# Optimization experiments

Hardware: AMD Instinct MI355X
Metric: run time of the kernel (lower is better)

The kernel has to match this reference:

```python
import jax, jax.numpy as jnp
import numpy as np

DELTA_VAR = 0.5
DELTA_DIST = 1.5
PULL_W = 1.0
PUSH_W = 1.0
REG_W = 0.001
IGNORE_INDEX = 255
NUM_IDS = 16  # max instance id used in setup; fixed segment count for jit


def setup_inputs() -> dict:
    key = jax.random.key(0)
    k1, k2 = jax.random.split(key)
    B, D, H, W = 8, 32, 512, 512
    pred_embedding = jax.random.normal(k1, (B, D, H, W), dtype=jnp.float32)
    gt_instance = jax.random.randint(k2, (B, H, W), 0, NUM_IDS).astype(jnp.int32)
    valid_mask = jnp.ones((B, H, W), dtype=bool)
    return {"pred_embedding": pred_embedding, "gt_instance": gt_instance, "valid_mask": valid_mask}


def _per_image(emb_hwd, inst_hw, vmask_hw):
    # emb_hwd: [H, W, D]; inst_hw, vmask_hw: [H, W]
    D = emb_hwd.shape[-1]
    e = emb_hwd.reshape(-1, D)                       # [N, D]
    inst = inst_hw.reshape(-1)
    m = (vmask_hw.reshape(-1)) & (inst != IGNORE_INDEX)
    mf = m.astype(e.dtype)
    # route invalid pixels to dummy segment NUM_IDS
    seg = jnp.where(m, inst, NUM_IDS)
    counts = jax.ops.segment_sum(mf, seg, num_segments=NUM_IDS + 1)[:NUM_IDS]      # [K]
    sums = jax.ops.segment_sum(e * mf[:, None], seg, num_segments=NUM_IDS + 1)[:NUM_IDS]  # [K, D]
    valid_id = counts > 0
    n_ids = jnp.sum(valid_id.astype(e.dtype))
    centers = sums / jnp.maximum(counts, 1.0)[:, None]                              # [K, D]
    # ---- pull: per-instance mean of relu(||pix - center|| - delta_var)^2 ----
    centers_full = jnp.concatenate([centers, jnp.zeros((1, D), e.dtype)], axis=0)   # dummy row
    c_pix = centers_full[seg]                                                        # [N, D]
    sq = jnp.sum((e - c_pix) ** 2, axis=-1)
    dist = jnp.sqrt(jnp.where(m, sq, 1.0))
    val = jnp.where(m, jax.nn.relu(dist - DELTA_VAR) ** 2, 0.0)
    per_inst = jax.ops.segment_sum(val, seg, num_segments=NUM_IDS + 1)[:NUM_IDS] / jnp.maximum(counts, 1.0)
    pull = jnp.sum(per_inst * valid_id.astype(e.dtype)) / jnp.maximum(n_ids, 1.0)
    # ---- push: pairwise relu(2*delta_dist - ||ci - cj||)^2, off-diagonal mean ----
    sqm = jnp.sum((centers[:, None, :] - centers[None, :, :]) ** 2, axis=-1)        # [K, K]
    eye = jnp.eye(NUM_IDS, dtype=bool)
    pmask = valid_id[:, None] & valid_id[None, :] & (~eye)
    dm = jnp.sqrt(jnp.where(pmask, sqm, 1.0))
    push_mat = jax.nn.relu(2.0 * DELTA_DIST - dm) ** 2
    n_pairs = jnp.sum(pmask.astype(e.dtype))
    push = jnp.where(n_ids > 1.0, jnp.sum(jnp.where(pmask, push_mat, 0.0)) / jnp.maximum(n_pairs, 1.0), 0.0)
    # ---- reg: mean center norm ----
    csq = jnp.sum(centers ** 2, axis=-1)
    cnorm = jnp.sqrt(jnp.where(valid_id, csq, 1.0))
    reg = jnp.sum(jnp.where(valid_id, cnorm, 0.0)) / jnp.maximum(n_ids, 1.0)
    vb = jnp.any(m).astype(e.dtype)
    return pull * vb, push * vb, reg * vb, vb


def reference(pred_embedding, gt_instance, valid_mask):
    emb = jnp.transpose(pred_embedding, (0, 2, 3, 1))  # [B, H, W, D]
    pulls, pushes, regs, vbs = jax.vmap(_per_image)(emb, gt_instance, valid_mask)
    nvb = jnp.sum(vbs)
    denom = jnp.maximum(nvb, 1.0)
    loss = (PULL_W * jnp.sum(pulls) + PUSH_W * jnp.sum(pushes) + REG_W * jnp.sum(regs)) / denom
    return jnp.where(nvb > 0, loss, 0.0)
```

## Files before the change

kernel.cpp:

```cpp
#include <hip/hip_runtime.h>

typedef _Float16 half4 __attribute__((ext_vector_type(4)));
typedef float f32x4 __attribute__((ext_vector_type(4)));

#define NB 8
#define ND 32
#define NHW (512*512)
#define NK 16
#define IGN 255

#define WS_S   1088
#define O_CNT  0
#define O_VPIX 16
#define O_SUM  32
#define O_PULL 1056

#define IDP_OFF 65536

#define ATPB 256
#define ABLK 128
#define TILE 128
#define NTILES 16

#define PTPB 256
#define PCHUNKS 256
#define PPIX (NHW / PCHUNKS)

__global__ __launch_bounds__(256) void k_zero(float* __restrict__ ws) {
    int i = blockIdx.x * blockDim.x + threadIdx.x;
    if (i < NB * WS_S) ws[i] = 0.f;
}

__global__ __launch_bounds__(ATPB) void k_accum(const float* __restrict__ pred,
                                                const int* __restrict__ inst,
                                                const unsigned char* __restrict__ msk,
                                                float* __restrict__ ws,
                                                unsigned char* __restrict__ idp) {
    __shared__ __align__(16) float buf[2][ND][TILE];
    __shared__ float lcnt[2][NK + 1];
    const int tid = threadIdx.x;
    const int w = tid >> 6, l = tid & 63;
    const int dgrp = w & 1;
    const int phalf = w >> 1;
    const int b = blockIdx.y, chunk = blockIdx.x;

    if (tid < 2 * (NK + 1)) ((float*)lcnt)[tid] = 0.f;

    const size_t img = (size_t)b * NHW;
    const float* pb = pred + (size_t)b * ND * NHW;
    const int base0 = chunk * (NTILES * TILE);

#define STAGE(CUR, T)                                                          \
    {                                                                          \
        const int tb_ = base0 + (T) * TILE;                                    \
        _Pragma("unroll")                                                      \
        for (int q_ = 0; q_ < 4; ++q_) {                                       \
            const int r0_ = 8 * w + 2 * q_;                                    \
            const int r_ = r0_ + (l >> 5);                                     \
            const int col_ = 4 * ((l & 31) ^ (r_ & 7));                        \
            const float* src_ = pb + (size_t)r_ * NHW + tb_ + col_;            \
            __builtin_amdgcn_global_load_lds(                                  \
                (const __attribute__((address_space(1))) unsigned*)src_,       \
                (__attribute__((address_space(3))) unsigned*)&buf[CUR][r0_][0],\
                16, 0, 0);                                                     \
        }                                                                      \
    }

#define LOADIDS(IV, MV, TB)                                                    \
    if (l < 16) {                                                              \
        (IV) = *(const int4*)(inst + img + (TB) + phalf * 64 + 4 * l);         \
        (MV) = *(const unsigned*)(msk + img + (TB) + phalf * 64 + 4 * l);      \
    }

#define DECODE(IV, MV, PK, VC)                                                 \
    if (l < 16) {                                                              \
        const int ia_[4] = {(IV).x, (IV).y, (IV).z, (IV).w};                   \
        (PK) = 0u;                                                             \
        _Pragma("unroll")                                                      \
        for (int p_ = 0; p_ < 4; ++p_) {                                       \
            const bool m_ = ((((MV) >> (8 * p_)) & 0xffu) != 0u) &&            \
                            (ia_[p_] != IGN);                                  \
            if (dgrp == 0) (VC) += m_ ? 1.f : 0.f;                             \
            const unsigned s_ =                                                \
                (m_ && (unsigned)ia_[p_] < NK) ? (unsigned)ia_[p_] : NK;       \
            (PK) |= s_ << (8 * p_);                                            \
        }                                                                      \
    }

    int4 iv; unsigned mv = 0;
    LOADIDS(iv, mv, base0);
    STAGE(0, 0);
    unsigned pk = 0;
    float vcnt = 0.f;
    DECODE(iv, mv, pk, vcnt);
    __syncthreads();

    f32x4 acc = {0.f, 0.f, 0.f, 0.f};
    for (int t = 0; t < NTILES; ++t) {
        const int cur = t & 1;
        const int tb = base0 + t * TILE;
        int4 iv2; unsigned mv2 = 0;
        if (t + 1 < NTILES) {
            LOADIDS(iv2, mv2, base0 + (t + 1) * TILE);
            STAGE(cur ^ 1, t + 1);
        }
        if (dgrp == 0 && l < 16) {
            uchar4 pkb = {(unsigned char)(pk & 0xff),
                          (unsigned char)((pk >> 8) & 0xff),
                          (unsigned char)((pk >> 16) & 0xff),
                          (unsigned char)(pk >> 24)};
            *(uchar4*)(idp + img + tb + phalf * 64 + 4 * l) = pkb;
            #pragma unroll
            for (int p = 0; p < 4; ++p)
                atomicAdd(&lcnt[phalf][(pk >> (8 * p)) & 0xffu], 1.f);
        }
        #pragma unroll
        for (int kk = 0; kk < 4; ++kk) {
            const int row = dgrp * 16 + (l & 15);
            const int cb = phalf * 16 + kk * 4 + (l >> 4);
            const f32x4 av = *(const f32x4*)
                (&buf[cur][0][0] + row * TILE + 4 * (cb ^ (row & 7)));
            half4 ah;
            #pragma unroll
            for (int e = 0; e < 4; ++e) ah[e] = (_Float16)av[e];
            const int srcl = kk * 4 + (l >> 4);
            const unsigned pkk = (unsigned)__shfl((int)pk, srcl);
            half4 bh;
            #pragma unroll
            for (int e = 0; e < 4; ++e)
                bh[e] = (((pkk >> (8 * e)) & 0xffu) == (unsigned)(l & 15))
                            ? (_Float16)1.f : (_Float16)0.f;
            acc = __builtin_amdgcn_mfma_f32_16x16x16f16(ah, bh, acc, 0, 0, 0);
        }
        iv = iv2; mv = mv2;
        DECODE(iv, mv, pk, vcnt);
        __syncthreads();
    }
#undef STAGE
#undef LOADIDS
#undef DECODE

    float* sc = &buf[0][0][0];
    const int widx = dgrp * 2 + phalf;
    #pragma unroll
    for (int r = 0; r < 4; ++r)
        sc[(widx * 16 + 4 * (l >> 4) + r) * 16 + (l & 15)] = acc[r];
    __syncthreads();

    float* wb = ws + b * WS_S;
    for (int i = tid; i < NK * ND; i += ATPB) {
        const int k = i >> 5, d = i & 31, dg = d >> 4, dr = d & 15;
        const float v = sc[((dg * 2 + 0) * 16 + dr) * 16 + k] +
                        sc[((dg * 2 + 1) * 16 + dr) * 16 + k];
        atomicAdd(&wb[O_SUM + i], v);
    }
    if (tid < NK) atomicAdd(&wb[O_CNT + tid], lcnt[0][tid] + lcnt[1][tid]);
    if (w == 0 || w == 2) {
        #pragma unroll
        for (int off = 8; off > 0; off >>= 1) vcnt += __shfl_down(vcnt, off);
        if (l == 0) atomicAdd(&wb[O_VPIX], vcnt);
    }
}

__global__ __launch_bounds__(PTPB) void k_pull(const float* __restrict__ pred,
                                               const unsigned char* __restrict__ idp,
                                               float* __restrict__ ws) {
    __shared__ float lc[17][ND + 1];
    __shared__ float lcc[NK];
    __shared__ float lp[2][NK];
    const int tid = threadIdx.x;
    const int b = NB - 1 - blockIdx.y;
    const int chunk = PCHUNKS - 1 - blockIdx.x;
    const int half = (tid >> 5) & 1;
    float* wb = ws + b * WS_S;

    if (tid < NK) lcc[tid] = wb[O_CNT + tid];
    if (tid < 2 * NK) ((float*)lp)[tid] = 0.f;
    __syncthreads();
    for (int i = tid; i < 17 * ND; i += PTPB)
        lc[i >> 5][i & 31] =
            (i < NK * ND) ? wb[O_SUM + i] / fmaxf(lcc[i >> 5], 1.f) : 0.f;
    __syncthreads();

    const size_t img = (size_t)b * NHW;
    const float* pb = pred + (size_t)b * ND * NHW;

    const int pix = chunk * PPIX + 4 * tid;
    const unsigned pk = *(const unsigned*)(idp + img + pix);
    const int id[4] = {(int)(pk & 0xff), (int)((pk >> 8) & 0xff),
                       (int)((pk >> 16) & 0xff), (int)(pk >> 24)};
    float sq[4] = {0.f, 0.f, 0.f, 0.f};
    #pragma unroll 8
    for (int d = 0; d < ND; ++d) {
        const float4 v = *(const float4*)(pb + (size_t)d * NHW + pix);
        float df0 = v.x - lc[id[0]][d];
        float df1 = v.y - lc[id[1]][d];
        float df2 = v.z - lc[id[2]][d];
        float df3 = v.w - lc[id[3]][d];
        sq[0] += df0 * df0; sq[1] += df1 * df1;
        sq[2] += df2 * df2; sq[3] += df3 * df3;
    }
    #pragma unroll
    for (int p = 0; p < 4; ++p) {
        if (id[p] < NK) {
            float r = fmaxf(sqrtf(sq[p]) - 0.5f, 0.f);
            atomicAdd(&lp[half][id[p]], r * r);
        }
    }
    __syncthreads();
    if (tid < NK) atomicAdd(&wb[O_PULL + tid], lp[0][tid] + lp[1][tid]);
}

__global__ void k_final(const float* __restrict__ ws, float* __restrict__ out) {
    __shared__ float lc[NK][ND];
    __shared__ float lcc[NK];
    const int tid = threadIdx.x;
    float total = 0.f, nvb = 0.f;

    for (int b = 0; b < NB; ++b) {
        const float* wb = ws + b * WS_S;
        if (tid < NK) lcc[tid] = wb[O_CNT + tid];
        __syncthreads();
        for (int i = tid; i < NK * ND; i += 64)
            lc[i >> 5][i & 31] = wb[O_SUM + i] / fmaxf(lcc[i >> 5], 1.f);
        __syncthreads();

        float nids_p = (tid < NK && lcc[tid] > 0.f) ? 1.f : 0.f;
        float pull_p = (tid < NK && lcc[tid] > 0.f)
                           ? wb[O_PULL + tid] / fmaxf(lcc[tid], 1.f) : 0.f;
        float reg_p = 0.f;
        if (tid < NK && lcc[tid] > 0.f) {
            float cs = 0.f;
            for (int d = 0; d < ND; ++d) cs += lc[tid][d] * lc[tid][d];
            reg_p = sqrtf(cs);
        }
        float push_p = 0.f;
        #pragma unroll
        for (int q = 0; q < 4; ++q) {
            const int p = 4 * tid + q, i = p >> 4, j = p & 15;
            if (i != j && lcc[i] > 0.f && lcc[j] > 0.f) {
                float sq2 = 0.f;
                for (int d = 0; d < ND; ++d) {
                    float df = lc[i][d] - lc[j][d];
                    sq2 += df * df;
                }
                float r = fmaxf(3.f - sqrtf(sq2), 0.f);
                push_p += r * r;
            }
        }
        #pragma unroll
        for (int off = 32; off > 0; off >>= 1) {
            nids_p += __shfl_down(nids_p, off);
            pull_p += __shfl_down(pull_p, off);
            reg_p  += __shfl_down(reg_p, off);
            push_p += __shfl_down(push_p, off);
        }
        if (tid == 0) {
            const float nids = nids_p;
            const float pull = pull_p / fmaxf(nids, 1.f);
            const float npairs = nids * nids - nids;
            const float push =
                (nids > 1.f) ? push_p / fmaxf(npairs, 1.f) : 0.f;
            const float reg = reg_p / fmaxf(nids, 1.f);
            const float vb = (wb[O_VPIX] > 0.f) ? 1.f : 0.f;
            total += (pull + push + 0.001f * reg) * vb;
            nvb += vb;
        }
        __syncthreads();
    }
    if (tid == 0) out[0] = (nvb > 0.f) ? total / fmaxf(nvb, 1.f) : 0.f;
}

extern "C" void kernel_launch(void* const* d_in, const int* in_sizes, int n_in,
                              void* d_out, int out_size, void* d_ws, size_t ws_size,
                              hipStream_t stream) {
    const float* pred = (const float*)d_in[0];
    const int* inst = (const int*)d_in[1];
    const unsigned char* msk = (const unsigned char*)d_in[2];
    float* out = (float*)d_out;
    float* ws = (float*)d_ws;
    unsigned char* idp = (unsigned char*)d_ws + IDP_OFF;

    k_zero<<<(NB * WS_S + 255) / 256, 256, 0, stream>>>(ws);
    dim3 agrid(ABLK, NB);
    k_accum<<<agrid, ATPB, 0, stream>>>(pred, inst, msk, ws, idp);
    dim3 pgrid(PCHUNKS, NB);
    k_pull<<<pgrid, PTPB, 0, stream>>>(pred, idp, ws);
    k_final<<<1, 64, 0, stream>>>(ws, out);
}
```

Before: 136.7 us.

## Give each wave a private tile slice and drop per-tile block barriers in accum

The accumulation kernel now gives each of the four waves its own 64-pixel slice of a 256-pixel tile, covering all 32 embedding dimensions with two MFMA accumulators. Because each wave only reads LDS it staged itself, the per-tile __syncthreads is replaced by explicit vmcnt waits, which removes block-wide barrier stalls. Tile size doubles and the block count halves (ABLK 64), so each block does more work with fewer blocks overall. The code relies on the exact vmcnt count matching the number of outstanding loads, so any change to the load pattern could cause it to read stale LDS data.

```diff
diff --git a/kernel.cpp b/kernel.cpp
--- a/kernel.cpp
+++ b/kernel.cpp
@@ -18,8 +18,8 @@
 #define IDP_OFF 65536
 
 #define ATPB 256
-#define ABLK 128
-#define TILE 128
+#define ABLK 64
+#define TILE 256
 #define NTILES 16
 
 #define PTPB 256
@@ -36,43 +36,44 @@
                                                 const unsigned char* __restrict__ msk,
                                                 float* __restrict__ ws,
                                                 unsigned char* __restrict__ idp) {
-    __shared__ __align__(16) float buf[2][ND][TILE];
-    __shared__ float lcnt[2][NK + 1];
+    __shared__ __align__(16) float buf[2][4][ND][64];
+    __shared__ float lcnt[4][20];
     const int tid = threadIdx.x;
     const int w = tid >> 6, l = tid & 63;
-    const int dgrp = w & 1;
-    const int phalf = w >> 1;
+    const int lq = l >> 4, lr = l & 15;
     const int b = blockIdx.y, chunk = blockIdx.x;
 
-    if (tid < 2 * (NK + 1)) ((float*)lcnt)[tid] = 0.f;
+    if (l < 20) lcnt[w][l] = 0.f;
 
     const size_t img = (size_t)b * NHW;
     const float* pb = pred + (size_t)b * ND * NHW;
     const int base0 = chunk * (NTILES * TILE);
+    const int sbase = 64 * w;
 
 #define STAGE(CUR, T)                                                          \
     {                                                                          \
-        const int tb_ = base0 + (T) * TILE;                                    \
+        const int tb_ = base0 + (T) * TILE + sbase;                            \
         _Pragma("unroll")                                                      \
-        for (int q_ = 0; q_ < 4; ++q_) {                                       \
-            const int r0_ = 8 * w + 2 * q_;                                    \
-            const int r_ = r0_ + (l >> 5);                                     \
-            const int col_ = 4 * ((l & 31) ^ (r_ & 7));                        \
-            const float* src_ = pb + (size_t)r_ * NHW + tb_ + col_;            \
+        for (int q_ = 0; q_ < 8; ++q_) {                                       \
+            const int r_ = 4 * q_ + lq;                                        \
+            const float* src_ =                                                \
+                pb + (size_t)r_ * NHW + tb_ + 4 * (lr ^ (r_ & 15));            \
             __builtin_amdgcn_global_load_lds(                                  \
                 (const __attribute__((address_space(1))) unsigned*)src_,       \
-                (__attribute__((address_space(3))) unsigned*)&buf[CUR][r0_][0],\
+                (__attribute__((address_space(3)))                             \
+                     unsigned*)&buf[CUR][w][4 * q_][0],                        \
                 16, 0, 0);                                                     \
         }                                                                      \
     }
 
-#define LOADIDS(IV, MV, TB)                                                    \
+#define LOADIDS(IV, MV, T)                                                     \
     if (l < 16) {                                                              \
-        (IV) = *(const int4*)(inst + img + (TB) + phalf * 64 + 4 * l);         \
-        (MV) = *(const unsigned*)(msk + img + (TB) + phalf * 64 + 4 * l);      \
-    }
-
-#define DECODE(IV, MV, PK, VC)                                                 \
+        const int tb_ = base0 + (T) * TILE + sbase;                            \
+        (IV) = *(const int4*)(inst + img + tb_ + 4 * l);                       \
+        (MV) = *(const unsigned*)(msk + img + tb_ + 4 * l);                    \
+    }
+
+#define DECODE(IV, MV, PK)                                                     \
     if (l < 16) {                                                              \
         const int ia_[4] = {(IV).x, (IV).y, (IV).z, (IV).w};                   \
         (PK) = 0u;                                                             \
@@ -80,86 +81,98 @@
         for (int p_ = 0; p_ < 4; ++p_) {                                       \
             const bool m_ = ((((MV) >> (8 * p_)) & 0xffu) != 0u) &&            \
                             (ia_[p_] != IGN);                                  \
-            if (dgrp == 0) (VC) += m_ ? 1.f : 0.f;                             \
+            vcnt += m_ ? 1.f : 0.f;                                            \
             const unsigned s_ =                                                \
                 (m_ && (unsigned)ia_[p_] < NK) ? (unsigned)ia_[p_] : NK;       \
             (PK) |= s_ << (8 * p_);                                            \
         }                                                                      \
     }
 
+    float vcnt = 0.f;
     int4 iv; unsigned mv = 0;
-    LOADIDS(iv, mv, base0);
+    LOADIDS(iv, mv, 0);
     STAGE(0, 0);
-    unsigned pk = 0;
-    float vcnt = 0.f;
-    DECODE(iv, mv, pk, vcnt);
-    __syncthreads();
-
-    f32x4 acc = {0.f, 0.f, 0.f, 0.f};
+
+    f32x4 acc0 = {0.f, 0.f, 0.f, 0.f};
+    f32x4 acc1 = {0.f, 0.f, 0.f, 0.f};
+
     for (int t = 0; t < NTILES; ++t) {
         const int cur = t & 1;
-        const int tb = base0 + t * TILE;
         int4 iv2; unsigned mv2 = 0;
         if (t + 1 < NTILES) {
-            LOADIDS(iv2, mv2, base0 + (t + 1) * TILE);
+            LOADIDS(iv2, mv2, t + 1);
             STAGE(cur ^ 1, t + 1);
-        }
-        if (dgrp == 0 && l < 16) {
+            asm volatile("s_waitcnt vmcnt(10)" ::: "memory");
+        } else {
+            asm volatile("s_waitcnt vmcnt(0)" ::: "memory");
+        }
+        __builtin_amdgcn_sched_barrier(0);
+
+        unsigned pk = 0;
+        DECODE(iv, mv, pk);
+        if (l < 16) {
             uchar4 pkb = {(unsigned char)(pk & 0xff),
                           (unsigned char)((pk >> 8) & 0xff),
                           (unsigned char)((pk >> 16) & 0xff),
                           (unsigned char)(pk >> 24)};
-            *(uchar4*)(idp + img + tb + phalf * 64 + 4 * l) = pkb;
+            *(uchar4*)(idp + img + base0 + t * TILE + sbase + 4 * l) = pkb;
             #pragma unroll
             for (int p = 0; p < 4; ++p)
-                atomicAdd(&lcnt[phalf][(pk >> (8 * p)) & 0xffu], 1.f);
-        }
+                atomicAdd(&lcnt[w][(pk >> (8 * p)) & 0xffu], 1.f);
+        }
+
+        const float* bufc = &buf[cur][w][0][0];
         #pragma unroll
         for (int kk = 0; kk < 4; ++kk) {
-            const int row = dgrp * 16 + (l & 15);
-            const int cb = phalf * 16 + kk * 4 + (l >> 4);
-            const f32x4 av = *(const f32x4*)
-                (&buf[cur][0][0] + row * TILE + 4 * (cb ^ (row & 7)));
-            half4 ah;
-            #pragma unroll
-            for (int e = 0; e < 4; ++e) ah[e] = (_Float16)av[e];
-            const int srcl = kk * 4 + (l >> 4);
-            const unsigned pkk = (unsigned)__shfl((int)pk, srcl);
+            const unsigned pkk = (unsigned)__shfl((int)pk, kk * 4 + lq);
             half4 bh;
             #pragma unroll
             for (int e = 0; e < 4; ++e)
-                bh[e] = (((pkk >> (8 * e)) & 0xffu) == (unsigned)(l & 15))
+                bh[e] = (((pkk >> (8 * e)) & 0xffu) == (unsigned)lr)
                             ? (_Float16)1.f : (_Float16)0.f;
-            acc = __builtin_amdgcn_mfma_f32_16x16x16f16(ah, bh, acc, 0, 0, 0);
+            const int cb = (kk * 4 + lq) ^ lr;
+            const f32x4 av0 = *(const f32x4*)(bufc + (size_t)lr * 64 + 4 * cb);
+            const f32x4 av1 =
+                *(const f32x4*)(bufc + (size_t)(16 + lr) * 64 + 4 * cb);
+            half4 ah0, ah1;
+            #pragma unroll
+            for (int e = 0; e < 4; ++e) {
+                ah0[e] = (_Float16)av0[e];
+                ah1[e] = (_Float16)av1[e];
+            }
+            acc0 = __builtin_amdgcn_mfma_f32_16x16x16f16(ah0, bh, acc0, 0, 0, 0);
+            acc1 = __builtin_amdgcn_mfma_f32_16x16x16f16(ah1, bh, acc1, 0, 0, 0);
         }
         iv = iv2; mv = mv2;
-        DECODE(iv, mv, pk, vcnt);
-        __syncthreads();
     }
 #undef STAGE
 #undef LOADIDS
 #undef DECODE
 
-    float* sc = &buf[0][0][0];
-    const int widx = dgrp * 2 + phalf;
+    __syncthreads();
+    float* sc = &buf[0][0][0][0];
     #pragma unroll
-    for (int r = 0; r < 4; ++r)
-        sc[(widx * 16 + 4 * (l >> 4) + r) * 16 + (l & 15)] = acc[r];
+    for (int r = 0; r < 4; ++r) {
+        sc[((w * 2 + 0) * 16 + 4 * lq + r) * 16 + lr] = acc0[r];
+        sc[((w * 2 + 1) * 16 + 4 * lq + r) * 16 + lr] = acc1[r];
+    }
     __syncthreads();
 
     float* wb = ws + b * WS_S;
     for (int i = tid; i < NK * ND; i += ATPB) {
         const int k = i >> 5, d = i & 31, dg = d >> 4, dr = d & 15;
-        const float v = sc[((dg * 2 + 0) * 16 + dr) * 16 + k] +
-                        sc[((dg * 2 + 1) * 16 + dr) * 16 + k];
+        float v = 0.f;
+        #pragma unroll
+        for (int ww = 0; ww < 4; ++ww)
+            v += sc[((ww * 2 + dg) * 16 + dr) * 16 + k];
         atomicAdd(&wb[O_SUM + i], v);
     }
-    if (tid < NK) atomicAdd(&wb[O_CNT + tid], lcnt[0][tid] + lcnt[1][tid]);
-    if (w == 0 || w == 2) {
-        #pragma unroll
-        for (int off = 8; off > 0; off >>= 1) vcnt += __shfl_down(vcnt, off);
-        if (l == 0) atomicAdd(&wb[O_VPIX], vcnt);
-    }
+    if (tid < NK)
+        atomicAdd(&wb[O_CNT + tid],
+                  lcnt[0][tid] + lcnt[1][tid] + lcnt[2][tid] + lcnt[3][tid]);
+    #pragma unroll
+    for (int off = 8; off > 0; off >>= 1) vcnt += __shfl_down(vcnt, off);
+    if (l == 0) atomicAdd(&wb[O_VPIX], vcnt);
 }
 
 __global__ __launch_bounds__(PTPB) void k_pull(const float* __restrict__ pred,
```

Result: no change. 135.5 us (-0.8%).
